# Kernel tuning notes

Hardware: AMD Instinct MI355X
Metric: run time of the kernel (lower is better)

## Reference

```python
import jax, jax.numpy as jnp
import numpy as np

HIDDEN = 1024
NUM_EXPERTS = 8
TOP_K = 2


def setup_inputs() -> dict:
    key = jax.random.key(0)
    k_x, k_r, k_w1, k_w2 = jax.random.split(key, 4)
    x = jax.random.normal(k_x, (4, 2048, HIDDEN), dtype=jnp.float32)
    # router: nn.Linear(hidden, num_experts, bias=False) -> weight [E, H]
    router_w = jax.random.normal(k_r, (NUM_EXPERTS, HIDDEN), dtype=jnp.float32) * (HIDDEN ** -0.5)
    # expert FFN: Linear(H, 2H) then Linear(2H, H), stored as [E, H, 2H] and [E, 2H, H]
    w1 = jax.random.normal(k_w1, (NUM_EXPERTS, HIDDEN, 2 * HIDDEN), dtype=jnp.float32) * (HIDDEN ** -0.5)
    w2 = jax.random.normal(k_w2, (NUM_EXPERTS, 2 * HIDDEN, HIDDEN), dtype=jnp.float32) * ((2 * HIDDEN) ** -0.5)
    return {"x": x, "router_w": router_w, "w1": w1, "w2": w2}


def reference(x, router_w, w1, w2):
    bsz, seq, hidden = x.shape
    tokens = x.reshape(-1, hidden)                      # [T, H]
    logits = tokens @ router_w.T                        # [T, E]
    topk_vals, topk_idx = jax.lax.top_k(logits, TOP_K)  # [T, K]
    weights = jax.nn.softmax(topk_vals, axis=-1)        # [T, K]
    # Dense all-experts FFN (exact GELU, matching torch nn.GELU default)
    h = jnp.einsum('td,edf->etf', tokens, w1)           # [E, T, 2H]
    h = jax.nn.gelu(h, approximate=False)
    out_all = jnp.einsum('etf,efd->etd', h, w2)         # [E, T, H]
    # Gather top-k expert outputs per token and weighted-combine
    out_ted = jnp.transpose(out_all, (1, 0, 2))         # [T, E, H]
    gathered = jnp.take_along_axis(out_ted, topk_idx[:, :, None], axis=1)  # [T, K, H]
    output = jnp.sum(weights[:, :, None] * gathered, axis=1)               # [T, H]
    return output.reshape(bsz, seq, hidden)
```

## Files before the change

### kernel.cpp

```cpp
#include <hip/hip_runtime.h>
#include <cstdint>
#include <cstddef>

#define T_TOKENS 8192
#define HID 1024
#define HID2 2048
#define NE 8

typedef unsigned short u16;
typedef unsigned int u32;
typedef __bf16 bf16x8 __attribute__((ext_vector_type(8)));
typedef float f32x4 __attribute__((ext_vector_type(4)));

__device__ __forceinline__ float bf2f(u16 u) {
    union { u32 i; float f; } x; x.i = ((u32)u) << 16; return x.f;
}
__device__ __forceinline__ u16 f2bf(float f) {
    union { float f; u32 i; } x; x.f = f;
    u32 r = x.i + 0x7fffu + ((x.i >> 16) & 1u);
    return (u16)(r >> 16);
}

__device__ __forceinline__ void cp16(const void* g, void* l) {
    __builtin_amdgcn_global_load_lds(
        (const __attribute__((address_space(1))) u32*)g,
        (__attribute__((address_space(3))) u32*)l,
        16, 0, 0);
}

__device__ __forceinline__ float gelu_f(float v) {
    float v2 = v * v;
    float t = fmaf(0.0713548162726f, v2, 1.59576912161f);
    float d = 1.0f + __expf(-v * t);
    return v * __builtin_amdgcn_rcpf(d);
}

__global__ __launch_bounds__(256) void router_kernel(
    const float* __restrict__ x, const float* __restrict__ rw,
    u16* __restrict__ xb,
    int* __restrict__ cnt, int* __restrict__ rowlist,
    int* __restrict__ tok_slots, float* __restrict__ tok_w)
{
    __shared__ int lbin[NE];
    __shared__ int gbase[NE];
    int tid = threadIdx.x;
    if (tid < NE) lbin[tid] = 0;
    __syncthreads();

    int wave = tid >> 6;
    int lane = tid & 63;
    int tg = lane >> 3, il = lane & 7;
    int t = blockIdx.x * 32 + wave * 8 + tg;

    const float* xrow = x + (size_t)t * HID;
    u16* xbrow = xb + (size_t)t * HID;

    float acc[NE];
#pragma unroll
    for (int e = 0; e < NE; e++) acc[e] = 0.f;

#pragma unroll 8
    for (int q = 0; q < 32; q++) {
        int c = il * 4 + 32 * q;
        float4 xv = *(const float4*)(xrow + c);
        u16 p[4] = { f2bf(xv.x), f2bf(xv.y), f2bf(xv.z), f2bf(xv.w) };
        *(uint2*)(xbrow + c) = *(const uint2*)p;
#pragma unroll
        for (int e = 0; e < NE; e++) {
            float4 rv = *(const float4*)(rw + (size_t)e * HID + c);
            acc[e] = fmaf(xv.x, rv.x, acc[e]);
            acc[e] = fmaf(xv.y, rv.y, acc[e]);
            acc[e] = fmaf(xv.z, rv.z, acc[e]);
            acc[e] = fmaf(xv.w, rv.w, acc[e]);
        }
    }
#pragma unroll
    for (int e = 0; e < NE; e++) {
        acc[e] += __shfl_xor(acc[e], 1, 64);
        acc[e] += __shfl_xor(acc[e], 2, 64);
        acc[e] += __shfl_xor(acc[e], 4, 64);
    }

    int i0 = 0, i1 = 0, ph0 = 0, ph1 = 0;
    float w0 = 0.f, w1 = 0.f;
    if (il == 0) {
        float v0 = -1e30f;
#pragma unroll
        for (int e = 0; e < NE; e++) if (acc[e] > v0) { v0 = acc[e]; i0 = e; }
        float v1 = -1e30f;
#pragma unroll
        for (int e = 0; e < NE; e++) if (e != i0 && acc[e] > v1) { v1 = acc[e]; i1 = e; }
        w0 = 1.0f / (1.0f + __expf(v1 - v0));
        w1 = 1.0f - w0;
        ph0 = atomicAdd(&lbin[i0], 1);
        ph1 = atomicAdd(&lbin[i1], 1);
    }
    __syncthreads();
    if (tid < NE) gbase[tid] = atomicAdd(&cnt[tid * 32], lbin[tid]);
    __syncthreads();
    if (il == 0) {
        int p0 = gbase[i0] + ph0;
        int p1 = gbase[i1] + ph1;
        rowlist[i0 * T_TOKENS + p0] = t;
        rowlist[i1 * T_TOKENS + p1] = t;
        tok_slots[t * 2 + 0] = (i0 << 16) | p0;
        tok_slots[t * 2 + 1] = (i1 << 16) | p1;
        tok_w[t * 2 + 0] = w0;
        tok_w[t * 2 + 1] = w1;
    }
}

#define BM 256
#define BN 256
#define BK 64
#define LDSE (BM * BK)

__global__ void offsets_kernel(const int* __restrict__ cnt,
                               int* __restrict__ off, int* __restrict__ cntc,
                               int* __restrict__ tmap, int* __restrict__ ntile)
{
    if (threadIdx.x == 0) {
        int s = 0, ti = 0;
        for (int e = 0; e < NE; e++) {
            int c = cnt[e * 32];
            off[e] = s; cntc[e] = c; s += c;
            int nmt = (c + BM - 1) / BM;
            for (int m = 0; m < nmt; m++) tmap[ti++] = (e << 16) | m;
        }
        ntile[0] = ti;
    }
}

__global__ __launch_bounds__(256) void convtrans_kernel(
    const float* __restrict__ in, u16* __restrict__ outp, int K, int N)
{
    __shared__ u16 tile[64][72];
    int e = blockIdx.z;
    const float* ip = in + (size_t)e * K * N;
    u16* op = outp + (size_t)e * K * N;
    int n0 = blockIdx.x * 64, k0 = blockIdx.y * 64;
    int t = threadIdx.x;

    int k = t >> 2;
    int nq = (t & 3) * 16;
    const float* src = ip + (size_t)(k0 + k) * N + n0 + nq;
#pragma unroll
    for (int q = 0; q < 4; q++) {
        float4 v = *(const float4*)(src + q * 4);
        tile[nq + q * 4 + 0][k] = f2bf(v.x);
        tile[nq + q * 4 + 1][k] = f2bf(v.y);
        tile[nq + q * 4 + 2][k] = f2bf(v.z);
        tile[nq + q * 4 + 3][k] = f2bf(v.w);
    }
    __syncthreads();

    int n = t >> 2;
    int kq = (t & 3) * 16;
    u16* dst = op + (size_t)(n0 + n) * K + k0 + kq;
    *(uint4*)(dst + 0) = *(const uint4*)&tile[n][kq + 0];
    *(uint4*)(dst + 8) = *(const uint4*)&tile[n][kq + 8];
}

__global__ __launch_bounds__(512, 2) void gemm1_kernel(
    const u16* __restrict__ xb, const u16* __restrict__ w1t,
    const int* __restrict__ cntc, const int* __restrict__ off,
    const int* __restrict__ rowlist, const int* __restrict__ tmap,
    const int* __restrict__ ntile, u16* __restrict__ hbuf)
{
    __shared__ u16 As[2][LDSE];
    __shared__ u16 Bs[2][LDSE];
    __shared__ int toks[BM];

    int bt = blockIdx.x;
    if (bt >= ntile[0]) return;
    int em = tmap[bt];
    int e = em >> 16, mt = em & 0xffff;
    int nt = blockIdx.y;
    int n_e = cntc[e];

    int tid = threadIdx.x;
    if (tid < BM) {
        int r = mt * BM + tid;
        if (r >= n_e) r = n_e - 1;
        toks[tid] = rowlist[e * T_TOKENS + r];
    }
    __syncthreads();

    int wv = tid >> 6, lane = tid & 63;
    int wm = (wv >> 2) * 128, wn = (wv & 3) * 64;
    int l15 = lane & 15, l4 = lane >> 4;
    int sr = lane >> 3, sc = lane & 7;

    const u16* w1e = w1t + ((size_t)e * HID2 + nt * BN) * HID;

    const u16* aptr[4]; const u16* bptr[4];
    u16* adst[4]; u16* bdst[4];
#pragma unroll
    for (int i = 0; i < 4; i++) {
        int m = wv * 32 + i * 8 + sr;
        int gq = sc ^ (m & 7);
        aptr[i] = xb + (size_t)toks[m] * HID + gq * 8;
        adst[i] = &As[0][m * BK + sc * 8];
        bptr[i] = w1e + (size_t)m * HID + gq * 8;
        bdst[i] = &Bs[0][m * BK + sc * 8];
    }

    f32x4 acc[8][4];
#pragma unroll
    for (int i = 0; i < 8; i++)
#pragma unroll
        for (int j = 0; j < 4; j++) acc[i][j] = (f32x4){0.f, 0.f, 0.f, 0.f};

#pragma unroll
    for (int i = 0; i < 4; i++) { cp16(aptr[i], adst[i]); cp16(bptr[i], bdst[i]); }
    asm volatile("s_waitcnt vmcnt(0)" ::: "memory");
    __syncthreads();

    int cur = 0;
    for (int kt = 0; kt < HID / BK; kt++) {
        if (kt + 1 < HID / BK) {
            int kb = (kt + 1) * BK;
            int bo = (cur ^ 1) * LDSE;
#pragma unroll
            for (int i = 0; i < 4; i++) {
                cp16(aptr[i] + kb, adst[i] + bo);
                cp16(bptr[i] + kb, bdst[i] + bo);
            }
        }
        const u16* Ab = As[cur];
        const u16* Bb = Bs[cur];
#pragma unroll
        for (int ks = 0; ks < 2; ks++) {
            bf16x8 af[8], bfr[4];
            int q = ks * 4 + l4;
#pragma unroll
            for (int i = 0; i < 8; i++) {
                int ra = wm + i * 16 + l15;
                af[i] = *(const bf16x8*)&Ab[ra * BK + ((q ^ (ra & 7)) << 3)];
            }
#pragma unroll
            for (int j = 0; j < 4; j++) {
                int rb = wn + j * 16 + l15;
                bfr[j] = *(const bf16x8*)&Bb[rb * BK + ((q ^ (rb & 7)) << 3)];
            }
            __builtin_amdgcn_s_setprio(1);
#pragma unroll
            for (int i = 0; i < 8; i++)
#pragma unroll
                for (int j = 0; j < 4; j++)
                    acc[i][j] = __builtin_amdgcn_mfma_f32_16x16x32_bf16(bfr[j], af[i], acc[i][j], 0, 0, 0);
            __builtin_amdgcn_s_setprio(0);
        }
        if (kt + 1 < HID / BK) asm volatile("s_waitcnt vmcnt(0)" ::: "memory");
        __syncthreads();
        cur ^= 1;
    }

    int base_row = off[e] + mt * BM;
#pragma unroll
    for (int i = 0; i < 8; i++) {
        int m = wm + i * 16 + l15;
        int r = mt * BM + m;
        if (r < n_e) {
            u16* orow = hbuf + (size_t)(base_row + m) * HID2 + nt * BN + wn + l4 * 4;
#pragma unroll
            for (int j = 0; j < 4; j++) {
                u16 p[4];
#pragma unroll
                for (int rg = 0; rg < 4; rg++) p[rg] = f2bf(gelu_f(acc[i][j][rg]));
                *(uint2*)(orow + j * 16) = *(const uint2*)p;
            }
        }
    }
}

__global__ __launch_bounds__(512, 2) void gemm2_kernel(
    const u16* __restrict__ hbuf, const u16* __restrict__ w2t,
    const int* __restrict__ cntc, const int* __restrict__ off,
    const int* __restrict__ tmap, const int* __restrict__ ntile,
    u16* __restrict__ ybuf)
{
    __shared__ u16 As[2][LDSE];
    __shared__ u16 Bs[2][LDSE];

    int bt = blockIdx.x;
    if (bt >= ntile[0]) return;
    int em = tmap[bt];
    int e = em >> 16, mt = em & 0xffff;
    int nt = blockIdx.y;
    int n_e = cntc[e];

    int tid = threadIdx.x;
    int wv = tid >> 6, lane = tid & 63;
    int wm = (wv >> 2) * 128, wn = (wv & 3) * 64;
    int l15 = lane & 15, l4 = lane >> 4;
    int sr = lane >> 3, sc = lane & 7;

    const u16* hrow = hbuf + (size_t)(off[e] + mt * BM) * HID2;
    const u16* w2e = w2t + ((size_t)e * HID + nt * BN) * HID2;

    const u16* aptr[4]; const u16* bptr[4];
    u16* adst[4]; u16* bdst[4];
#pragma unroll
    for (int i = 0; i < 4; i++) {
        int m = wv * 32 + i * 8 + sr;
        int gq = sc ^ (m & 7);
        aptr[i] = hrow + (size_t)m * HID2 + gq * 8;
        adst[i] = &As[0][m * BK + sc * 8];
        bptr[i] = w2e + (size_t)m * HID2 + gq * 8;
        bdst[i] = &Bs[0][m * BK + sc * 8];
    }

    f32x4 acc[8][4];
#pragma unroll
    for (int i = 0; i < 8; i++)
#pragma unroll
        for (int j = 0; j < 4; j++) acc[i][j] = (f32x4){0.f, 0.f, 0.f, 0.f};

#pragma unroll
    for (int i = 0; i < 4; i++) { cp16(aptr[i], adst[i]); cp16(bptr[i], bdst[i]); }
    asm volatile("s_waitcnt vmcnt(0)" ::: "memory");
    __syncthreads();

    int cur = 0;
    for (int kt = 0; kt < HID2 / BK; kt++) {
        if (kt + 1 < HID2 / BK) {
            int kb = (kt + 1) * BK;
            int bo = (cur ^ 1) * LDSE;
#pragma unroll
            for (int i = 0; i < 4; i++) {
                cp16(aptr[i] + kb, adst[i] + bo);
                cp16(bptr[i] + kb, bdst[i] + bo);
            }
        }
        const u16* Ab = As[cur];
        const u16* Bb = Bs[cur];
#pragma unroll
        for (int ks = 0; ks < 2; ks++) {
            bf16x8 af[8], bfr[4];
            int q = ks * 4 + l4;
#pragma unroll
            for (int i = 0; i < 8; i++) {
                int ra = wm + i * 16 + l15;
                af[i] = *(const bf16x8*)&Ab[ra * BK + ((q ^ (ra & 7)) << 3)];
            }
#pragma unroll
            for (int j = 0; j < 4; j++) {
                int rb = wn + j * 16 + l15;
                bfr[j] = *(const bf16x8*)&Bb[rb * BK + ((q ^ (rb & 7)) << 3)];
            }
            __builtin_amdgcn_s_setprio(1);
#pragma unroll
            for (int i = 0; i < 8; i++)
#pragma unroll
                for (int j = 0; j < 4; j++)
                    acc[i][j] = __builtin_amdgcn_mfma_f32_16x16x32_bf16(bfr[j], af[i], acc[i][j], 0, 0, 0);
            __builtin_amdgcn_s_setprio(0);
        }
        if (kt + 1 < HID2 / BK) asm volatile("s_waitcnt vmcnt(0)" ::: "memory");
        __syncthreads();
        cur ^= 1;
    }

    int base_row = off[e] + mt * BM;
#pragma unroll
    for (int i = 0; i < 8; i++) {
        int m = wm + i * 16 + l15;
        int r = mt * BM + m;
        if (r < n_e) {
            u16* orow = ybuf + (size_t)(base_row + m) * HID + nt * BN + wn + l4 * 4;
#pragma unroll
            for (int j = 0; j < 4; j++) {
                u16 p[4];
#pragma unroll
                for (int rg = 0; rg < 4; rg++) p[rg] = f2bf(acc[i][j][rg]);
                *(uint2*)(orow + j * 16) = *(const uint2*)p;
            }
        }
    }
}

__global__ __launch_bounds__(256) void combine_kernel(
    const u16* __restrict__ ybuf, const int* __restrict__ off,
    const int* __restrict__ tok_slots, const float* __restrict__ tok_w,
    float* __restrict__ out)
{
    int tid = threadIdx.x;
    int t = blockIdx.x * 2 + (tid >> 7);
    int c = (tid & 127) * 8;
    int s0 = tok_slots[t * 2], s1 = tok_slots[t * 2 + 1];
    float w0 = tok_w[t * 2], w1 = tok_w[t * 2 + 1];
    int r0 = off[s0 >> 16] + (s0 & 0xFFFF);
    int r1 = off[s1 >> 16] + (s1 & 0xFFFF);
    uint4 a = *(const uint4*)(ybuf + (size_t)r0 * HID + c);
    uint4 b = *(const uint4*)(ybuf + (size_t)r1 * HID + c);
    const u16* pa = (const u16*)&a;
    const u16* pb = (const u16*)&b;
    float o[8];
#pragma unroll
    for (int q = 0; q < 8; q++) o[q] = w0 * bf2f(pa[q]) + w1 * bf2f(pb[q]);
    *(float4*)(out + (size_t)t * HID + c) = *(const float4*)&o[0];
    *(float4*)(out + (size_t)t * HID + c + 4) = *(const float4*)&o[4];
}

extern "C" void kernel_launch(void* const* d_in, const int* in_sizes, int n_in,
                              void* d_out, int out_size, void* d_ws, size_t ws_size,
                              hipStream_t stream)
{
    const float* x  = (const float*)d_in[0];
    const float* rw = (const float*)d_in[1];
    const float* w1 = (const float*)d_in[2];
    const float* w2 = (const float*)d_in[3];
    float* out = (float*)d_out;

    char* ws = (char*)d_ws;
    int*   cnt       = (int*)(ws + 0);
    int*   off       = (int*)(ws + 1024);
    int*   cntc      = (int*)(ws + 1088);
    int*   tmap      = (int*)(ws + 1152);
    int*   ntile     = (int*)(ws + 1536);
    int*   rowlist   = (int*)(ws + 2048);
    int*   tok_slots = (int*)(ws + 2048 + 262144);
    float* tok_w     = (float*)(ws + 2048 + 262144 + 65536);
    u16*   xb        = (u16*)(ws + (1ull << 20));
    u16*   wt        = (u16*)(ws + (17ull << 20));
    u16*   hbuf      = (u16*)(ws + (49ull << 20));
    u16*   ybuf      = (u16*)(ws + (114ull << 20));

    hipMemsetAsync(cnt, 0, 1024, stream);

    router_kernel<<<T_TOKENS / 32, 256, 0, stream>>>(x, rw, xb, cnt, rowlist, tok_slots, tok_w);
    offsets_kernel<<<1, 64, 0, stream>>>(cnt, off, cntc, tmap, ntile);

    convtrans_kernel<<<dim3(HID2 / 64, HID / 64, NE), 256, 0, stream>>>(w1, wt, HID, HID2);
    gemm1_kernel<<<dim3(72, HID2 / BN, 1), 512, 0, stream>>>(xb, wt, cntc, off, rowlist, tmap, ntile, hbuf);

    convtrans_kernel<<<dim3(HID / 64, HID2 / 64, NE), 256, 0, stream>>>(w2, wt, HID2, HID);
    gemm2_kernel<<<dim3(72, HID / BN, 1), 512, 0, stream>>>(hbuf, wt, cntc, off, tmap, ntile, ybuf);

    combine_kernel<<<T_TOKENS / 2, 256, 0, stream>>>(ybuf, off, tok_slots, tok_w, out);
}
```

Measured before the change: 485.0 us.

## Split GEMM K-tiles into halves with interleaved loads and XCD-aware block swizzle

```diff
diff --git a/kernel.cpp b/kernel.cpp
--- a/kernel.cpp
+++ b/kernel.cpp
@@ -34,6 +34,12 @@
     float d = 1.0f + __expf(-v * t);
     return v * __builtin_amdgcn_rcpf(d);
 }
+
+#define BAR()   asm volatile("s_barrier" ::: "memory")
+#define LGKM0() asm volatile("s_waitcnt lgkmcnt(0)" ::: "memory")
+#define VMC(n)  asm volatile("s_waitcnt vmcnt(" #n ")" ::: "memory")
+
+__device__ __forceinline__ int sfun(int r) { return (r & 2) | ((r >> 2) & 1); }
 
 __global__ __launch_bounds__(256) void router_kernel(
     const float* __restrict__ x, const float* __restrict__ rw,
@@ -113,7 +119,7 @@
 #define BM 256
 #define BN 256
 #define BK 64
-#define LDSE (BM * BK)
+#define HLF 8192
 
 __global__ void offsets_kernel(const int* __restrict__ cnt,
                                int* __restrict__ off, int* __restrict__ cntc,
@@ -167,15 +173,16 @@
     const int* __restrict__ rowlist, const int* __restrict__ tmap,
     const int* __restrict__ ntile, u16* __restrict__ hbuf)
 {
-    __shared__ u16 As[2][LDSE];
-    __shared__ u16 Bs[2][LDSE];
+    __shared__ u16 AsF[4 * HLF];
+    __shared__ u16 BsF[4 * HLF];
     __shared__ int toks[BM];
 
-    int bt = blockIdx.x;
+    int id = blockIdx.x;
+    int swz = (id & 7) * 72 + (id >> 3);
+    int bt = swz >> 3, nt = swz & 7;
     if (bt >= ntile[0]) return;
     int em = tmap[bt];
     int e = em >> 16, mt = em & 0xffff;
-    int nt = blockIdx.y;
     int n_e = cntc[e];
 
     int tid = threadIdx.x;
@@ -189,21 +196,25 @@
     int wv = tid >> 6, lane = tid & 63;
     int wm = (wv >> 2) * 128, wn = (wv & 3) * 64;
     int l15 = lane & 15, l4 = lane >> 4;
-    int sr = lane >> 3, sc = lane & 7;
-
-    const u16* w1e = w1t + ((size_t)e * HID2 + nt * BN) * HID;
-
-    const u16* aptr[4]; const u16* bptr[4];
-    u16* adst[4]; u16* bdst[4];
-#pragma unroll
-    for (int i = 0; i < 4; i++) {
-        int m = wv * 32 + i * 8 + sr;
-        int gq = sc ^ (m & 7);
-        aptr[i] = xb + (size_t)toks[m] * HID + gq * 8;
-        adst[i] = &As[0][m * BK + sc * 8];
-        bptr[i] = w1e + (size_t)m * HID + gq * 8;
-        bdst[i] = &Bs[0][m * BK + sc * 8];
-    }
+
+    int r0 = (wv * 2 + 0) * 16 + (lane >> 2);
+    int r1 = (wv * 2 + 1) * 16 + (lane >> 2);
+    int sl = lane & 3;
+    int as0 = (sl ^ sfun(r0)) << 3;
+    int as1 = (sl ^ sfun(r1)) << 3;
+    int d0 = (wv * 2 + 0) * 512 + lane * 8;
+    int d1 = (wv * 2 + 1) * 512 + lane * 8;
+    const u16* aRow0 = xb + (size_t)toks[r0] * HID;
+    const u16* aRow1 = xb + (size_t)toks[r1] * HID;
+    const u16* w1e = w1t + ((size_t)e * HID2 + (size_t)nt * BN) * HID;
+    const u16* bRow0 = w1e + (size_t)r0 * HID;
+    const u16* bRow1 = w1e + (size_t)r1 * HID;
+
+    int aoff[8], boff[4];
+#pragma unroll
+    for (int i = 0; i < 8; i++) { int ra = wm + i * 16 + l15; aoff[i] = ra * 32 + ((l4 ^ sfun(ra)) << 3); }
+#pragma unroll
+    for (int j = 0; j < 4; j++) { int rb = wn + j * 16 + l15; boff[j] = rb * 32 + ((l4 ^ sfun(rb)) << 3); }
 
     f32x4 acc[8][4];
 #pragma unroll
@@ -211,50 +222,82 @@
 #pragma unroll
         for (int j = 0; j < 4; j++) acc[i][j] = (f32x4){0.f, 0.f, 0.f, 0.f};
 
-#pragma unroll
-    for (int i = 0; i < 4; i++) { cp16(aptr[i], adst[i]); cp16(bptr[i], bdst[i]); }
-    asm volatile("s_waitcnt vmcnt(0)" ::: "memory");
-    __syncthreads();
-
-    int cur = 0;
-    for (int kt = 0; kt < HID / BK; kt++) {
-        if (kt + 1 < HID / BK) {
-            int kb = (kt + 1) * BK;
-            int bo = (cur ^ 1) * LDSE;
-#pragma unroll
-            for (int i = 0; i < 4; i++) {
-                cp16(aptr[i] + kb, adst[i] + bo);
-                cp16(bptr[i] + kb, bdst[i] + bo);
-            }
-        }
-        const u16* Ab = As[cur];
-        const u16* Bb = Bs[cur];
-#pragma unroll
-        for (int ks = 0; ks < 2; ks++) {
-            bf16x8 af[8], bfr[4];
-            int q = ks * 4 + l4;
-#pragma unroll
-            for (int i = 0; i < 8; i++) {
-                int ra = wm + i * 16 + l15;
-                af[i] = *(const bf16x8*)&Ab[ra * BK + ((q ^ (ra & 7)) << 3)];
-            }
-#pragma unroll
-            for (int j = 0; j < 4; j++) {
-                int rb = wn + j * 16 + l15;
-                bfr[j] = *(const bf16x8*)&Bb[rb * BK + ((q ^ (rb & 7)) << 3)];
-            }
-            __builtin_amdgcn_s_setprio(1);
-#pragma unroll
-            for (int i = 0; i < 8; i++)
-#pragma unroll
-                for (int j = 0; j < 4; j++)
-                    acc[i][j] = __builtin_amdgcn_mfma_f32_16x16x32_bf16(bfr[j], af[i], acc[i][j], 0, 0, 0);
-            __builtin_amdgcn_s_setprio(0);
-        }
-        if (kt + 1 < HID / BK) asm volatile("s_waitcnt vmcnt(0)" ::: "memory");
-        __syncthreads();
-        cur ^= 1;
-    }
+#define ST_A(db, h, kt) do { \
+    cp16(aRow0 + (kt) * BK + (h) * 32 + as0, &AsF[((db) * 2 + (h)) * HLF + d0]); \
+    cp16(aRow1 + (kt) * BK + (h) * 32 + as1, &AsF[((db) * 2 + (h)) * HLF + d1]); } while (0)
+#define ST_B(db, h, kt) do { \
+    cp16(bRow0 + (kt) * BK + (h) * 32 + as0, &BsF[((db) * 2 + (h)) * HLF + d0]); \
+    cp16(bRow1 + (kt) * BK + (h) * 32 + as1, &BsF[((db) * 2 + (h)) * HLF + d1]); } while (0)
+
+    const int NKT = HID / BK;
+    ST_A(0, 0, 0); ST_B(0, 0, 0);
+    ST_A(0, 1, 0); ST_B(0, 1, 0);
+    ST_A(1, 0, 1); ST_B(1, 0, 1);
+    VMC(4);
+    BAR();
+
+    for (int kt = 0; kt < NKT; kt++) {
+        int buf = kt & 1, nbuf = buf ^ 1;
+        int base0 = (buf * 2 + 0) * HLF;
+        int base1 = (buf * 2 + 1) * HLF;
+        bf16x8 af[8], bq0, bq1;
+#pragma unroll
+        for (int i = 0; i < 8; i++) af[i] = *(const bf16x8*)&AsF[base0 + aoff[i]];
+        bq0 = *(const bf16x8*)&BsF[base0 + boff[0]];
+        bq1 = *(const bf16x8*)&BsF[base0 + boff[1]];
+        if (kt + 1 < NKT) ST_A(nbuf, 1, kt + 1);
+        BAR(); LGKM0();
+        __builtin_amdgcn_s_setprio(1);
+#pragma unroll
+        for (int i = 0; i < 8; i++) {
+            acc[i][0] = __builtin_amdgcn_mfma_f32_16x16x32_bf16(bq0, af[i], acc[i][0], 0, 0, 0);
+            acc[i][1] = __builtin_amdgcn_mfma_f32_16x16x32_bf16(bq1, af[i], acc[i][1], 0, 0, 0);
+        }
+        __builtin_amdgcn_s_setprio(0);
+        BAR();
+        bq0 = *(const bf16x8*)&BsF[base0 + boff[2]];
+        bq1 = *(const bf16x8*)&BsF[base0 + boff[3]];
+        if (kt + 1 < NKT) ST_B(nbuf, 1, kt + 1);
+        BAR(); LGKM0();
+        __builtin_amdgcn_s_setprio(1);
+#pragma unroll
+        for (int i = 0; i < 8; i++) {
+            acc[i][2] = __builtin_amdgcn_mfma_f32_16x16x32_bf16(bq0, af[i], acc[i][2], 0, 0, 0);
+            acc[i][3] = __builtin_amdgcn_mfma_f32_16x16x32_bf16(bq1, af[i], acc[i][3], 0, 0, 0);
+        }
+        __builtin_amdgcn_s_setprio(0);
+        BAR();
+#pragma unroll
+        for (int i = 0; i < 8; i++) af[i] = *(const bf16x8*)&AsF[base1 + aoff[i]];
+        bq0 = *(const bf16x8*)&BsF[base1 + boff[0]];
+        bq1 = *(const bf16x8*)&BsF[base1 + boff[1]];
+        if (kt + 2 < NKT) ST_A(buf, 0, kt + 2);
+        BAR(); LGKM0();
+        __builtin_amdgcn_s_setprio(1);
+#pragma unroll
+        for (int i = 0; i < 8; i++) {
+            acc[i][0] = __builtin_amdgcn_mfma_f32_16x16x32_bf16(bq0, af[i], acc[i][0], 0, 0, 0);
+            acc[i][1] = __builtin_amdgcn_mfma_f32_16x16x32_bf16(bq1, af[i], acc[i][1], 0, 0, 0);
+        }
+        __builtin_amdgcn_s_setprio(0);
+        BAR();
+        bq0 = *(const bf16x8*)&BsF[base1 + boff[2]];
+        bq1 = *(const bf16x8*)&BsF[base1 + boff[3]];
+        if (kt + 2 < NKT) ST_B(buf, 0, kt + 2);
+        BAR(); LGKM0();
+        __builtin_amdgcn_s_setprio(1);
+#pragma unroll
+        for (int i = 0; i < 8; i++) {
+            acc[i][2] = __builtin_amdgcn_mfma_f32_16x16x32_bf16(bq0, af[i], acc[i][2], 0, 0, 0);
+            acc[i][3] = __builtin_amdgcn_mfma_f32_16x16x32_bf16(bq1, af[i], acc[i][3], 0, 0, 0);
+        }
+        __builtin_amdgcn_s_setprio(0);
+        if (kt + 2 < NKT)      { VMC(4); }
+        else if (kt + 1 < NKT) { VMC(0); }
+        BAR();
+    }
+#undef ST_A
+#undef ST_B
 
     int base_row = off[e] + mt * BM;
 #pragma unroll
@@ -280,36 +323,41 @@
     const int* __restrict__ tmap, const int* __restrict__ ntile,
     u16* __restrict__ ybuf)
 {
-    __shared__ u16 As[2][LDSE];
-    __shared__ u16 Bs[2][LDSE];
-
-    int bt = blockIdx.x;
+    __shared__ u16 AsF[4 * HLF];
+    __shared__ u16 BsF[4 * HLF];
+
+    int id = blockIdx.x;
+    int swz = (id & 7) * 36 + (id >> 3);
+    int bt = swz >> 2, nt = swz & 3;
     if (bt >= ntile[0]) return;
     int em = tmap[bt];
     int e = em >> 16, mt = em & 0xffff;
-    int nt = blockIdx.y;
     int n_e = cntc[e];
 
     int tid = threadIdx.x;
     int wv = tid >> 6, lane = tid & 63;
     int wm = (wv >> 2) * 128, wn = (wv & 3) * 64;
     int l15 = lane & 15, l4 = lane >> 4;
-    int sr = lane >> 3, sc = lane & 7;
-
+
+    int r0 = (wv * 2 + 0) * 16 + (lane >> 2);
+    int r1 = (wv * 2 + 1) * 16 + (lane >> 2);
+    int sl = lane & 3;
+    int as0 = (sl ^ sfun(r0)) << 3;
+    int as1 = (sl ^ sfun(r1)) << 3;
+    int d0 = (wv * 2 + 0) * 512 + lane * 8;
+    int d1 = (wv * 2 + 1) * 512 + lane * 8;
     const u16* hrow = hbuf + (size_t)(off[e] + mt * BM) * HID2;
-    const u16* w2e = w2t + ((size_t)e * HID + nt * BN) * HID2;
-
-    const u16* aptr[4]; const u16* bptr[4];
-    u16* adst[4]; u16* bdst[4];
-#pragma unroll
-    for (int i = 0; i < 4; i++) {
-        int m = wv * 32 + i * 8 + sr;
-        int gq = sc ^ (m & 7);
-        aptr[i] = hrow + (size_t)m * HID2 + gq * 8;
-        adst[i] = &As[0][m * BK + sc * 8];
-        bptr[i] = w2e + (size_t)m * HID2 + gq * 8;
-        bdst[i] = &Bs[0][m * BK + sc * 8];
-    }
+    const u16* aRow0 = hrow + (size_t)r0 * HID2;
+    const u16* aRow1 = hrow + (size_t)r1 * HID2;
+    const u16* w2e = w2t + ((size_t)e * HID + (size_t)nt * BN) * HID2;
+    const u16* bRow0 = w2e + (size_t)r0 * HID2;
+    const u16* bRow1 = w2e + (size_t)r1 * HID2;
+
+    int aoff[8], boff[4];
+#pragma unroll
+    for (int i = 0; i < 8; i++) { int ra = wm + i * 16 + l15; aoff[i] = ra * 32 + ((l4 ^ sfun(ra)) << 3); }
+#pragma unroll
+    for (int j = 0; j < 4; j++) { int rb = wn + j * 16 + l15; boff[j] = rb * 32 + ((l4 ^ sfun(rb)) << 3); }
 
     f32x4 acc[8][4];
 #pragma unroll
@@ -317,50 +365,82 @@
 #pragma unroll
         for (int j = 0; j < 4; j++) acc[i][j] = (f32x4){0.f, 0.f, 0.f, 0.f};
 
-#pragma unroll
-    for (int i = 0; i < 4; i++) { cp16(aptr[i], adst[i]); cp16(bptr[i], bdst[i]); }
-    asm volatile("s_waitcnt vmcnt(0)" ::: "memory");
-    __syncthreads();
-
-    int cur = 0;
-    for (int kt = 0; kt < HID2 / BK; kt++) {
-        if (kt + 1 < HID2 / BK) {
-            int kb = (kt + 1) * BK;
-            int bo = (cur ^ 1) * LDSE;
-#pragma unroll
-            for (int i = 0; i < 4; i++) {
-                cp16(aptr[i] + kb, adst[i] + bo);
-                cp16(bptr[i] + kb, bdst[i] + bo);
-            }
-        }
-        const u16* Ab = As[cur];
-        const u16* Bb = Bs[cur];
-#pragma unroll
-        for (int ks = 0; ks < 2; ks++) {
-            bf16x8 af[8], bfr[4];
-            int q = ks * 4 + l4;
-#pragma unroll
-            for (int i = 0; i < 8; i++) {
-                int ra = wm + i * 16 + l15;
-                af[i] = *(const bf16x8*)&Ab[ra * BK + ((q ^ (ra & 7)) << 3)];
-            }
-#pragma unroll
-            for (int j = 0; j < 4; j++) {
-                int rb = wn + j * 16 + l15;
-                bfr[j] = *(const bf16x8*)&Bb[rb * BK + ((q ^ (rb & 7)) << 3)];
-            }
-            __builtin_amdgcn_s_setprio(1);
-#pragma unroll
-            for (int i = 0; i < 8; i++)
-#pragma unroll
-                for (int j = 0; j < 4; j++)
-                    acc[i][j] = __builtin_amdgcn_mfma_f32_16x16x32_bf16(bfr[j], af[i], acc[i][j], 0, 0, 0);
-            __builtin_amdgcn_s_setprio(0);
-        }
-        if (kt + 1 < HID2 / BK) asm volatile("s_waitcnt vmcnt(0)" ::: "memory");
-        __syncthreads();
-        cur ^= 1;
-    }
+#define ST_A(db, h, kt) do { \
+    cp16(aRow0 + (kt) * BK + (h) * 32 + as0, &AsF[((db) * 2 + (h)) * HLF + d0]); \
+    cp16(aRow1 + (kt) * BK + (h) * 32 + as1, &AsF[((db) * 2 + (h)) * HLF + d1]); } while (0)
+#define ST_B(db, h, kt) do { \
+    cp16(bRow0 + (kt) * BK + (h) * 32 + as0, &BsF[((db) * 2 + (h)) * HLF + d0]); \
+    cp16(bRow1 + (kt) * BK + (h) * 32 + as1, &BsF[((db) * 2 + (h)) * HLF + d1]); } while (0)
+
+    const int NKT = HID2 / BK;
+    ST_A(0, 0, 0); ST_B(0, 0, 0);
+    ST_A(0, 1, 0); ST_B(0, 1, 0);
+    ST_A(1, 0, 1); ST_B(1, 0, 1);
+    VMC(4);
+    BAR();
+
+    for (int kt = 0; kt < NKT; kt++) {
+        int buf = kt & 1, nbuf = buf ^ 1;
+        int base0 = (buf * 2 + 0) * HLF;
+        int base1 = (buf * 2 + 1) * HLF;
+        bf16x8 af[8], bq0, bq1;
+#pragma unroll
+        for (int i = 0; i < 8; i++) af[i] = *(const bf16x8*)&AsF[base0 + aoff[i]];
+        bq0 = *(const bf16x8*)&BsF[base0 + boff[0]];
+        bq1 = *(const bf16x8*)&BsF[base0 + boff[1]];
+        if (kt + 1 < NKT) ST_A(nbuf, 1, kt + 1);
+        BAR(); LGKM0();
+        __builtin_amdgcn_s_setprio(1);
+#pragma unroll
+        for (int i = 0; i < 8; i++) {
+            acc[i][0] = __builtin_amdgcn_mfma_f32_16x16x32_bf16(bq0, af[i], acc[i][0], 0, 0, 0);
+            acc[i][1] = __builtin_amdgcn_mfma_f32_16x16x32_bf16(bq1, af[i], acc[i][1], 0, 0, 0);
+        }
+        __builtin_amdgcn_s_setprio(0);
+        BAR();
+        bq0 = *(const bf16x8*)&BsF[base0 + boff[2]];
+        bq1 = *(const bf16x8*)&BsF[base0 + boff[3]];
+        if (kt + 1 < NKT) ST_B(nbuf, 1, kt + 1);
+        BAR(); LGKM0();
+        __builtin_amdgcn_s_setprio(1);
+#pragma unroll
+        for (int i = 0; i < 8; i++) {
+            acc[i][2] = __builtin_amdgcn_mfma_f32_16x16x32_bf16(bq0, af[i], acc[i][2], 0, 0, 0);
+            acc[i][3] = __builtin_amdgcn_mfma_f32_16x16x32_bf16(bq1, af[i], acc[i][3], 0, 0, 0);
+        }
+        __builtin_amdgcn_s_setprio(0);
+        BAR();
+#pragma unroll
+        for (int i = 0; i < 8; i++) af[i] = *(const bf16x8*)&AsF[base1 + aoff[i]];
+        bq0 = *(const bf16x8*)&BsF[base1 + boff[0]];
+        bq1 = *(const bf16x8*)&BsF[base1 + boff[1]];
+        if (kt + 2 < NKT) ST_A(buf, 0, kt + 2);
+        BAR(); LGKM0();
+        __builtin_amdgcn_s_setprio(1);
+#pragma unroll
+        for (int i = 0; i < 8; i++) {
+            acc[i][0] = __builtin_amdgcn_mfma_f32_16x16x32_bf16(bq0, af[i], acc[i][0], 0, 0, 0);
+            acc[i][1] = __builtin_amdgcn_mfma_f32_16x16x32_bf16(bq1, af[i], acc[i][1], 0, 0, 0);
+        }
+        __builtin_amdgcn_s_setprio(0);
+        BAR();
+        bq0 = *(const bf16x8*)&BsF[base1 + boff[2]];
+        bq1 = *(const bf16x8*)&BsF[base1 + boff[3]];
+        if (kt + 2 < NKT) ST_B(buf, 0, kt + 2);
+        BAR(); LGKM0();
+        __builtin_amdgcn_s_setprio(1);
+#pragma unroll
+        for (int i = 0; i < 8; i++) {
+            acc[i][2] = __builtin_amdgcn_mfma_f32_16x16x32_bf16(bq0, af[i], acc[i][2], 0, 0, 0);
+            acc[i][3] = __builtin_amdgcn_mfma_f32_16x16x32_bf16(bq1, af[i], acc[i][3], 0, 0, 0);
+        }
+        __builtin_amdgcn_s_setprio(0);
+        if (kt + 2 < NKT)      { VMC(4); }
+        else if (kt + 1 < NKT) { VMC(0); }
+        BAR();
+    }
+#undef ST_A
+#undef ST_B
 
     int base_row = off[e] + mt * BM;
 #pragma unroll
@@ -433,10 +513,10 @@
     offsets_kernel<<<1, 64, 0, stream>>>(cnt, off, cntc, tmap, ntile);
 
     convtrans_kernel<<<dim3(HID2 / 64, HID / 64, NE), 256, 0, stream>>>(w1, wt, HID, HID2);
-    gemm1_kernel<<<dim3(72, HID2 / BN, 1), 512, 0, stream>>>(xb, wt, cntc, off, rowlist, tmap, ntile, hbuf);
+    gemm1_kernel<<<72 * (HID2 / BN), 512, 0, stream>>>(xb, wt, cntc, off, rowlist, tmap, ntile, hbuf);
 
     convtrans_kernel<<<dim3(HID / 64, HID2 / 64, NE), 256, 0, stream>>>(w2, wt, HID2, HID);
-    gemm2_kernel<<<dim3(72, HID / BN, 1), 512, 0, stream>>>(hbuf, wt, cntc, off, tmap, ntile, ybuf);
+    gemm2_kernel<<<72 * (HID / BN), 512, 0, stream>>>(hbuf, wt, cntc, off, tmap, ntile, ybuf);
 
     combine_kernel<<<T_TOKENS / 2, 256, 0, stream>>>(ybuf, off, tok_slots, tok_w, out);
 }
```

Result: no change. 477.3 us (-1.6%).
